# Performance work log

Measured on AMD Instinct MI355X. Metric: run time of the kernel, lower is better.

The kernel has to match this reference:

```python
import jax, jax.numpy as jnp
import numpy as np

ATTN_SCALE = 0.12  # attn_args.attn_scale (constant hyperparameter)
EPS = 1e-6         # F.rms_norm eps
GATE_IN = 12       # attn_gate input features (x[..., :12])


def rms_norm(x):
    return x * jax.lax.rsqrt(jnp.mean(x * x, axis=-1, keepdims=True) + EPS)


def rotary(x, cos, sin):
    # x: [B,T,H,D]; cos/sin: [T,D//2]
    x1, x2 = jnp.split(x, 2, axis=-1)
    c = cos[None, :, None, :]
    s = sin[None, :, None, :]
    return jnp.concatenate([x1 * c + x2 * s, -x1 * s + x2 * c], axis=-1)


def setup_inputs() -> dict:
    key = jax.random.key(0)
    ks = jax.random.split(key, 5)
    B, T, D, H, HD = 1, 2048, 1024, 8, 128
    std = 0.5 * D ** -0.5
    x = jax.random.normal(ks[0], (B, T, D), jnp.float32)
    qkvo_w = jax.random.normal(ks[1], (4, D, D), jnp.float32) * std
    gate_w = jax.random.normal(ks[2], (H, GATE_IN), jnp.float32) * 0.02
    ve = jax.random.normal(ks[3], (B, T, H, HD), jnp.float32)
    sa_lambdas = jax.random.uniform(ks[4], (2,), jnp.float32, 0.3, 0.7)
    half = HD // 2
    inv_freq = 1.0 / (10000.0 ** (jnp.arange(half, dtype=jnp.float32) / half))
    ang = jnp.arange(T, dtype=jnp.float32)[:, None] * inv_freq[None, :]
    return dict(x=x, qkvo_w=qkvo_w, gate_w=gate_w, ve=ve,
                sa_lambdas=sa_lambdas, cos=jnp.cos(ang), sin=jnp.sin(ang))


def reference(x, qkvo_w, gate_w, ve, sa_lambdas, cos, sin):
    B, T, D = x.shape
    H = gate_w.shape[0]
    HD = D // H
    # fused QKV projection: rows of qkvo_w[:3] are [q; k; v]
    w_qkv = qkvo_w[:3].reshape(3 * D, D)           # [3D, D]
    qkv = jnp.einsum('btd,ed->bte', x, w_qkv)      # [B,T,3D]
    qkv = qkv.reshape(B, T, 3, H, HD)
    q, k, v = qkv[:, :, 0], qkv[:, :, 1], qkv[:, :, 2]
    # RMSNorm + RoPE on q, k
    q = rotary(rms_norm(q), cos, sin)
    k = rotary(rms_norm(k), cos, sin)
    # value-residual mixing
    v = sa_lambdas[0] * v + sa_lambdas[1] * ve
    # causal SDPA with custom scale
    scores = jnp.einsum('bqhd,bkhd->bhqk', q, k) * ATTN_SCALE
    causal = jnp.tril(jnp.ones((T, T), dtype=bool))
    scores = jnp.where(causal[None, None], scores, jnp.finfo(scores.dtype).min)
    p = jax.nn.softmax(scores, axis=-1)
    y = jnp.einsum('bhqk,bkhd->bqhd', p, v)        # [B,T,H,HD]
    # per-head sigmoid gate from the first 12 channels of x
    gate = jax.nn.sigmoid(jnp.einsum('bti,hi->bth', x[..., :GATE_IN], gate_w))
    y = y * gate[..., None]
    # output projection (qkvo_w[3]): F.linear -> y @ W_o^T
    out = jnp.einsum('bti,oi->bto', y.reshape(B, T, H * HD), qkvo_w[3])
    return out
```

## Files before the change

kernel.cpp:

```cpp
#include <hip/hip_runtime.h>
#include <stdint.h>

typedef unsigned short u16;
typedef unsigned int u32;

typedef __bf16 bfx8 __attribute__((ext_vector_type(8)));
typedef float fx4 __attribute__((ext_vector_type(4)));
typedef float fx16 __attribute__((ext_vector_type(16)));
typedef u16 u16x4 __attribute__((ext_vector_type(4)));
typedef u16 u16x8 __attribute__((ext_vector_type(8)));

#define GAS __attribute__((address_space(1)))
#define LAS __attribute__((address_space(3)))

__device__ __forceinline__ void gload16(const void* g, void* l) {
  __builtin_amdgcn_global_load_lds((GAS void*)g, (LAS void*)l, 16, 0, 0);
}

__device__ __forceinline__ u16 f2bf(float f) {
  union { float f; u32 u; } v; v.f = f;
  u32 r = v.u + 0x7fffu + ((v.u >> 16) & 1u);
  return (u16)(r >> 16);
}
__device__ __forceinline__ float bf2f(u16 u) {
  union { u32 u; float f; } v; v.u = ((u32)u) << 16;
  return v.f;
}

__global__ __launch_bounds__(256) void k_cvt(const float* __restrict__ src, u16* __restrict__ dst, int n) {
  int i = (blockIdx.x * 256 + threadIdx.x) * 8;
  if (i >= n) return;
  const float4* s = (const float4*)(src + i);
  float4 a = s[0], b = s[1];
  u16x8 o;
  o[0] = f2bf(a.x); o[1] = f2bf(a.y); o[2] = f2bf(a.z); o[3] = f2bf(a.w);
  o[4] = f2bf(b.x); o[5] = f2bf(b.y); o[6] = f2bf(b.z); o[7] = f2bf(b.w);
  *(u16x8*)(dst + i) = o;
}

__global__ __launch_bounds__(256) void k_gemm_out(const u16* __restrict__ A, const u16* __restrict__ B,
                                                  float* __restrict__ C, int M, int N, int K) {
  __shared__ char sm[16384];
  const int tid = threadIdx.x;
  const int l = tid & 63, w = tid >> 6;
  const int li = l & 15, lg = l >> 4;
  const int nbm = M >> 6;
  const int bm = blockIdx.x % nbm, bn = blockIdx.x / nbm;

  const u16* gsrc[4];
#pragma unroll
  for (int i = 0; i < 4; ++i) {
    int b = i * 4096 + tid * 16;
    int row, ch;
    const u16* mat;
    if (b < 8192) { row = b >> 7; mat = A + (size_t)(bm * 64 + row) * K; }
    else          { int bb = b - 8192; row = bb >> 7; mat = B + (size_t)(bn * 64 + row) * K; }
    ch = ((b >> 4) & 7) ^ (row & 7);
    gsrc[i] = mat + ch * 8;
  }

  fx4 acc[4];
#pragma unroll
  for (int jj = 0; jj < 4; ++jj)
#pragma unroll
    for (int r = 0; r < 4; ++r) acc[jj][r] = 0.f;

  for (int k0 = 0; k0 < K; k0 += 64) {
    __syncthreads();
#pragma unroll
    for (int i = 0; i < 4; ++i) gload16(gsrc[i] + k0, sm + i * 4096 + w * 1024);
    __syncthreads();
#pragma unroll
    for (int kk = 0; kk < 2; ++kk) {
      int rowa = w * 16 + li;
      bfx8 af = *(const bfx8*)(sm + rowa * 128 + (((kk * 4 + lg)) ^ (rowa & 7)) * 16);
#pragma unroll
      for (int nf = 0; nf < 4; ++nf) {
        int rowb = nf * 16 + li;
        bfx8 bfr = *(const bfx8*)(sm + 8192 + rowb * 128 + ((kk * 4 + lg) ^ (rowb & 7)) * 16);
        acc[nf] = __builtin_amdgcn_mfma_f32_16x16x32_bf16(af, bfr, acc[nf], 0, 0, 0);
      }
    }
  }
#pragma unroll
  for (int nf = 0; nf < 4; ++nf)
#pragma unroll
    for (int r = 0; r < 4; ++r) {
      int row = bm * 64 + w * 16 + lg * 4 + r;
      int col = bn * 64 + nf * 16 + li;
      C[(size_t)row * N + col] = acc[nf][r];
    }
}

__global__ __launch_bounds__(256) void k_gemm_qkv(const u16* __restrict__ A, const u16* __restrict__ B,
                                                  u16* __restrict__ qkv, u16* __restrict__ vt,
                                                  const float* __restrict__ ve, const float* __restrict__ lam,
                                                  const float* __restrict__ cosp, const float* __restrict__ sinp) {
  __shared__ char sm[24576];
  const int tid = threadIdx.x;
  const int l = tid & 63, w = tid >> 6;
  const int li = l & 15, lg = l >> 4;
  const int bm = blockIdx.x & 31, bn = blockIdx.x >> 5;
  const int K = 1024;

  const u16* gsrc[6];
#pragma unroll
  for (int i = 0; i < 6; ++i) {
    int b = i * 4096 + tid * 16;
    int row, ch;
    const u16* mat;
    if (b < 8192) { row = b >> 7; mat = A + (size_t)(bm * 64 + row) * K; }
    else          { int bb = b - 8192; row = bb >> 7; mat = B + (size_t)(bn * 128 + row) * K; }
    ch = ((b >> 4) & 7) ^ (row & 7);
    gsrc[i] = mat + ch * 8;
  }

  fx4 acc[8];
#pragma unroll
  for (int jj = 0; jj < 8; ++jj)
#pragma unroll
    for (int r = 0; r < 4; ++r) acc[jj][r] = 0.f;

  for (int k0 = 0; k0 < K; k0 += 64) {
    __syncthreads();
#pragma unroll
    for (int i = 0; i < 6; ++i) gload16(gsrc[i] + k0, sm + i * 4096 + w * 1024);
    __syncthreads();
#pragma unroll
    for (int kk = 0; kk < 2; ++kk) {
      int rowa = w * 16 + li;
      bfx8 af = *(const bfx8*)(sm + rowa * 128 + ((kk * 4 + lg) ^ (rowa & 7)) * 16);
#pragma unroll
      for (int nf = 0; nf < 8; ++nf) {
        int rowb = nf * 16 + li;
        bfx8 bfr = *(const bfx8*)(sm + 8192 + rowb * 128 + ((kk * 4 + lg) ^ (rowb & 7)) * 16);
        acc[nf] = __builtin_amdgcn_mfma_f32_16x16x32_bf16(af, bfr, acc[nf], 0, 0, 0);
      }
    }
  }

  const int s = bn >> 3, h = bn & 7;
  if (s < 2) {
#pragma unroll
    for (int r = 0; r < 4; ++r) {
      int t = bm * 64 + w * 16 + lg * 4 + r;
      float ss = 0.f;
#pragma unroll
      for (int nf = 0; nf < 8; ++nf) ss += acc[nf][r] * acc[nf][r];
      ss += __shfl_xor(ss, 1); ss += __shfl_xor(ss, 2);
      ss += __shfl_xor(ss, 4); ss += __shfl_xor(ss, 8);
      float rn = rsqrtf(ss * (1.f / 128.f) + 1e-6f);
      u16* qp = qkv + (size_t)t * 3072 + s * 1024 + h * 128;
#pragma unroll
      for (int nf = 0; nf < 4; ++nf) {
        int dp = nf * 16 + li;
        float c = cosp[(size_t)t * 64 + dp];
        float sn = sinp[(size_t)t * 64 + dp];
        float x1 = acc[nf][r] * rn, x2 = acc[nf + 4][r] * rn;
        qp[dp] = f2bf(x1 * c + x2 * sn);
        qp[dp + 64] = f2bf(-x1 * sn + x2 * c);
      }
    }
  } else {
    const float l0 = lam[0], l1 = lam[1];
    int tb = bm * 64 + w * 16 + lg * 4;
#pragma unroll
    for (int nf = 0; nf < 8; ++nf) {
      int d = nf * 16 + li;
      u16x4 o;
#pragma unroll
      for (int r = 0; r < 4; ++r)
        o[r] = f2bf(l0 * acc[nf][r] + l1 * ve[(size_t)(tb + r) * 1024 + h * 128 + d]);
      *(u16x4*)(vt + (size_t)h * 262144 + (size_t)d * 2048 + tb) = o;
    }
  }
}

__global__ __launch_bounds__(256) void k_attn2(const u16* __restrict__ qkv, const u16* __restrict__ vt,
                                               float* __restrict__ part, float* __restrict__ ml) {
  __shared__ char sm[32768];
  const int bid = blockIdx.x;
  const int h = bid / 40;
  const int r40 = bid % 40;
  const int g = (r40 < 4) ? 0 : (r40 < 12) ? 1 : (r40 < 24) ? 2 : 3;
  const int Gt = (g == 0) ? 0 : (g == 1) ? 4 : (g == 2) ? 12 : 24;
  const int nseg = g + 1;
  const int idx = r40 - Gt;
  const int qb = g * 4 + idx / nseg;
  const int s = idx % nseg;
  const int q0 = qb * 128;
  const int seg0 = s * 512;
  const int seg_len = min(512, (qb + 1) * 128 - seg0);
  const int nkt = seg_len >> 5;

  const int tid = threadIdx.x;
  const int l = tid & 63, w = tid >> 6;
  const int li = l & 31, hi = l >> 5;
  const int qrow = q0 + w * 32 + li;
  const int wqmax = q0 + w * 32 + 31;
  const int wqmin = q0 + w * 32;

  bfx8 Q[8];
  {
    const u16* qp = qkv + (size_t)qrow * 3072 + h * 128 + hi * 8;
#pragma unroll
    for (int c = 0; c < 8; ++c) Q[c] = *(const bfx8*)(qp + c * 16);
  }

  const u16* kbase = qkv + 1024 + h * 128;
  const u16* vbase = vt + (size_t)h * 262144;

  auto STAGE = [&](int kt, int buf) {
    const int kabs = seg0 + kt * 32;
    char* dst = sm + buf * 16384;
#pragma unroll
    for (int i = 0; i < 2; ++i) {
      int j = w * 2 + i;
      int row = j * 4 + (l >> 4);
      int ch = (l & 15) ^ (row & 7);
      gload16(kbase + (size_t)(kabs + row) * 3072 + ch * 8, dst + j * 1024);
    }
#pragma unroll
    for (int i = 0; i < 2; ++i) {
      int j = w * 2 + i;
      int d = (j & 1) * 64 + l;
      int slot = j >> 1;
      gload16(vbase + (size_t)d * 2048 + kabs + slot * 8, dst + 8192 + j * 1024);
    }
  };

  fx16 Y[4];
#pragma unroll
  for (int d = 0; d < 4; ++d)
#pragma unroll
    for (int r = 0; r < 16; ++r) Y[d][r] = 0.f;
  float m_run = -1e30f, l_run = 0.f;

  STAGE(0, 0);
  __syncthreads();
  int cur = 0;

  for (int kt = 0; kt < nkt; ++kt) {
    if (kt + 1 < nkt) STAGE(kt + 1, cur ^ 1);
    const int k0 = seg0 + kt * 32;
    if (k0 <= wqmax) {
      const char* kb = sm + cur * 16384;
      const char* vb = kb + 8192;
      fx16 S;
#pragma unroll
      for (int r = 0; r < 16; ++r) S[r] = 0.f;
#pragma unroll
      for (int c = 0; c < 8; ++c) {
        int ch = (c * 2 + hi) ^ (li & 7);
        bfx8 kf = *(const bfx8*)(kb + li * 256 + ch * 16);
        S = __builtin_amdgcn_mfma_f32_32x32x16_bf16(kf, Q[c], S, 0, 0, 0);
      }
      const bool nomask = (k0 + 31 <= wqmin);
      float p[16];
      float mt = -1e30f;
#pragma unroll
      for (int r = 0; r < 16; ++r) {
        int kk = (r & 3) + 8 * (r >> 2) + 4 * hi;
        float sv = (nomask || (k0 + kk <= qrow)) ? S[r] * 0.12f : -1e30f;
        p[r] = sv;
        mt = fmaxf(mt, sv);
      }
      mt = fmaxf(mt, __shfl_xor(mt, 32));
      float mnew = fmaxf(m_run, mt);
      float alpha = __expf(m_run - mnew);
      float ssum = 0.f;
#pragma unroll
      for (int r = 0; r < 16; ++r) { float e = __expf(p[r] - mnew); p[r] = e; ssum += e; }
      ssum += __shfl_xor(ssum, 32);
      l_run = l_run * alpha + ssum;
      m_run = mnew;
#pragma unroll
      for (int d = 0; d < 4; ++d)
#pragma unroll
        for (int r = 0; r < 16; ++r) Y[d][r] *= alpha;
      u32 pk[8], pks[8];
#pragma unroll
      for (int i = 0; i < 8; ++i) pk[i] = (u32)f2bf(p[2 * i]) | ((u32)f2bf(p[2 * i + 1]) << 16);
#pragma unroll
      for (int i = 0; i < 8; ++i) pks[i] = (u32)__shfl_xor((int)pk[i], 32);
      union { u32 u[4]; bfx8 v; } P0, P1;
      if (hi == 0) {
        P0.u[0] = pk[0];  P0.u[1] = pk[1];  P0.u[2] = pks[0]; P0.u[3] = pks[1];
        P1.u[0] = pk[4];  P1.u[1] = pk[5];  P1.u[2] = pks[4]; P1.u[3] = pks[5];
      } else {
        P0.u[0] = pks[2]; P0.u[1] = pks[3]; P0.u[2] = pk[2];  P0.u[3] = pk[3];
        P1.u[0] = pks[6]; P1.u[1] = pks[7]; P1.u[2] = pk[6];  P1.u[3] = pk[7];
      }
#pragma unroll
      for (int db = 0; db < 4; ++db) {
        int dd = db * 32 + li;
        bfx8 v0 = *(const bfx8*)(vb + hi * 2048 + dd * 16);
        bfx8 v1 = *(const bfx8*)(vb + (2 + hi) * 2048 + dd * 16);
        Y[db] = __builtin_amdgcn_mfma_f32_32x32x16_bf16(v0, P0.v, Y[db], 0, 0, 0);
        Y[db] = __builtin_amdgcn_mfma_f32_32x32x16_bf16(v1, P1.v, Y[db], 0, 0, 0);
      }
    }
    __syncthreads();
    cur ^= 1;
  }

  if (hi == 0) {
    ml[(size_t)bid * 256 + (w * 32 + li) * 2 + 0] = m_run;
    ml[(size_t)bid * 256 + (w * 32 + li) * 2 + 1] = l_run;
  }
  float* Yl = (float*)(sm + w * 8192);
  float* pdst = part + (size_t)bid * 16384;
#pragma unroll
  for (int P = 0; P < 2; ++P) {
    asm volatile("" ::: "memory");
#pragma unroll
    for (int dh = 0; dh < 2; ++dh) {
      int db = P * 2 + dh;
#pragma unroll
      for (int r = 0; r < 16; ++r) {
        int dloc = dh * 32 + (r & 3) + 8 * (r >> 2) + 4 * hi;
        Yl[li * 64 + (dloc ^ ((li & 7) << 2))] = Y[db][r];
      }
    }
    asm volatile("" ::: "memory");
    int rr = l >> 1, c0 = (l & 1) * 32, sx = (rr & 7) << 2;
#pragma unroll
    for (int j = 0; j < 8; ++j) {
      float4 v = *(const float4*)(Yl + rr * 64 + ((c0 + j * 4) ^ sx));
      *(float4*)(pdst + (w * 32 + rr) * 128 + P * 64 + c0 + j * 4) = v;
    }
  }
}

__global__ __launch_bounds__(256) void k_comb(const float* __restrict__ part, const float* __restrict__ ml,
                                              const float* __restrict__ x, const float* __restrict__ gw,
                                              u16* __restrict__ y) {
  const int b = blockIdx.x;
  const int h = b >> 4, qb = b & 15;
  const int g = qb >> 2;
  const int nseg = g + 1;
  const int Gt = (g == 0) ? 0 : (g == 1) ? 4 : (g == 2) ? 12 : 24;
  const int slot0 = h * 40 + Gt + (qb & 3) * nseg;
  const int t = threadIdx.x;
  const int r = t >> 1, hf = (t & 1) * 64;
  const int q = qb * 128 + r;

  float ms[4], ls[4];
  float M = -1e30f;
#pragma unroll
  for (int s = 0; s < 4; ++s) {
    if (s < nseg) {
      ms[s] = ml[(size_t)(slot0 + s) * 256 + r * 2 + 0];
      ls[s] = ml[(size_t)(slot0 + s) * 256 + r * 2 + 1];
      M = fmaxf(M, ms[s]);
    }
  }
  float wt[4];
  float L = 0.f;
#pragma unroll
  for (int s = 0; s < 4; ++s) {
    if (s < nseg) { wt[s] = __expf(ms[s] - M); L += wt[s] * ls[s]; }
  }
  float4 acc[16];
#pragma unroll
  for (int j = 0; j < 16; ++j) { acc[j].x = 0.f; acc[j].y = 0.f; acc[j].z = 0.f; acc[j].w = 0.f; }
#pragma unroll
  for (int s = 0; s < 4; ++s) {
    if (s < nseg) {
      const float4* P = (const float4*)(part + (size_t)(slot0 + s) * 16384 + r * 128 + hf);
      float ws_ = wt[s];
#pragma unroll
      for (int j = 0; j < 16; ++j) {
        float4 v = P[j];
        acc[j].x += ws_ * v.x; acc[j].y += ws_ * v.y; acc[j].z += ws_ * v.z; acc[j].w += ws_ * v.w;
      }
    }
  }
  float dot = 0.f;
#pragma unroll
  for (int i = 0; i < 12; ++i) dot += x[(size_t)q * 1024 + i] * gw[h * 12 + i];
  float gt_ = 1.f / (1.f + __expf(-dot));
  float sc = gt_ / L;
  u16* yp = y + (size_t)q * 1024 + h * 128 + hf;
#pragma unroll
  for (int j = 0; j < 8; ++j) {
    float4 a = acc[2 * j], bb = acc[2 * j + 1];
    u16x8 o;
    o[0] = f2bf(a.x * sc); o[1] = f2bf(a.y * sc); o[2] = f2bf(a.z * sc); o[3] = f2bf(a.w * sc);
    o[4] = f2bf(bb.x * sc); o[5] = f2bf(bb.y * sc); o[6] = f2bf(bb.z * sc); o[7] = f2bf(bb.w * sc);
    *(u16x8*)(yp + j * 8) = o;
  }
}

extern "C" void kernel_launch(void* const* d_in, const int* in_sizes, int n_in,
                              void* d_out, int out_size, void* d_ws, size_t ws_size,
                              hipStream_t stream) {
  const float* x = (const float*)d_in[0];
  const float* qkvo_w = (const float*)d_in[1];
  const float* gate_w = (const float*)d_in[2];
  const float* ve = (const float*)d_in[3];
  const float* lam = (const float*)d_in[4];
  const float* cosp = (const float*)d_in[5];
  const float* sinp = (const float*)d_in[6];
  float* out = (float*)d_out;

  u16* wb  = (u16*)d_ws;
  u16* xb  = wb + 4u * 1024 * 1024;
  u16* qkv = xb + 2u * 1024 * 1024;
  u16* vt  = qkv + 6u * 1024 * 1024;
  u16* y   = vt + 2u * 1024 * 1024;
  float* part = (float*)((char*)d_ws + (size_t)32 * 1024 * 1024);
  float* ml = part + (size_t)320 * 16384;

  k_cvt<<<dim3(2048), dim3(256), 0, stream>>>(qkvo_w, wb, 4 * 1024 * 1024);
  k_cvt<<<dim3(1024), dim3(256), 0, stream>>>(x, xb, 2 * 1024 * 1024);
  k_gemm_qkv<<<dim3(32 * 24), dim3(256), 0, stream>>>(xb, wb, qkv, vt, ve, lam, cosp, sinp);
  k_attn2<<<dim3(320), dim3(256), 0, stream>>>(qkv, vt, part, ml);
  k_comb<<<dim3(128), dim3(256), 0, stream>>>(part, ml, x, gate_w, y);
  k_gemm_out<<<dim3(32 * 16), dim3(256), 0, stream>>>(y, wb + 3u * 1024 * 1024, out, 2048, 1024, 1024);
}
```

Measured before the change: 101.9 us.

## Split attention KV into 256-key segments, store partials in bf16, remap blocks per XCD

Attention work is split into 256-key segments instead of 512, giving 576 blocks instead of 320 for better load balance across CUs. A closed-form segment index replaces the group tables. Partial outputs are stored as bf16 to halve partial traffic, and the combine kernel merges up to 8 segments. Block IDs in both GEMMs and the attention kernel are remapped so consecutive tiles land on the same XCD for L2 reuse. In exchange, bf16 partials lose precision and the combine step reads more segments.

```diff
diff --git a/kernel.cpp b/kernel.cpp
--- a/kernel.cpp
+++ b/kernel.cpp
@@ -26,6 +26,8 @@
   union { u32 u; float f; } v; v.u = ((u32)u) << 16;
   return v.f;
 }
+
+__device__ __forceinline__ int segF(int qb) { return (qb * qb + 2 * qb + (qb & 1)) >> 2; }
 
 __global__ __launch_bounds__(256) void k_cvt(const float* __restrict__ src, u16* __restrict__ dst, int n) {
   int i = (blockIdx.x * 256 + threadIdx.x) * 8;
@@ -44,8 +46,9 @@
   const int tid = threadIdx.x;
   const int l = tid & 63, w = tid >> 6;
   const int li = l & 15, lg = l >> 4;
+  const int bid = (blockIdx.x & 7) * 64 + (blockIdx.x >> 3);
   const int nbm = M >> 6;
-  const int bm = blockIdx.x % nbm, bn = blockIdx.x / nbm;
+  const int bm = bid % nbm, bn = bid / nbm;
 
   const u16* gsrc[4];
 #pragma unroll
@@ -100,7 +103,8 @@
   const int tid = threadIdx.x;
   const int l = tid & 63, w = tid >> 6;
   const int li = l & 15, lg = l >> 4;
-  const int bm = blockIdx.x & 31, bn = blockIdx.x >> 5;
+  const int bid = (blockIdx.x & 7) * 96 + (blockIdx.x >> 3);
+  const int bm = bid & 31, bn = bid >> 5;
   const int K = 1024;
 
   const u16* gsrc[6];
@@ -177,20 +181,17 @@
 }
 
 __global__ __launch_bounds__(256) void k_attn2(const u16* __restrict__ qkv, const u16* __restrict__ vt,
-                                               float* __restrict__ part, float* __restrict__ ml) {
+                                               u16* __restrict__ part, float* __restrict__ ml) {
   __shared__ char sm[32768];
-  const int bid = blockIdx.x;
-  const int h = bid / 40;
-  const int r40 = bid % 40;
-  const int g = (r40 < 4) ? 0 : (r40 < 12) ? 1 : (r40 < 24) ? 2 : 3;
-  const int Gt = (g == 0) ? 0 : (g == 1) ? 4 : (g == 2) ? 12 : 24;
-  const int nseg = g + 1;
-  const int idx = r40 - Gt;
-  const int qb = g * 4 + idx / nseg;
-  const int s = idx % nseg;
+  const int bid = (blockIdx.x & 7) * 72 + (blockIdx.x >> 3);
+  const int h = bid / 72;
+  const int r72 = bid % 72;
+  int qb = 15;
+  while (segF(qb) > r72) --qb;
+  const int s = r72 - segF(qb);
   const int q0 = qb * 128;
-  const int seg0 = s * 512;
-  const int seg_len = min(512, (qb + 1) * 128 - seg0);
+  const int seg0 = s * 256;
+  const int seg_len = min(256, (qb + 1) * 128 - seg0);
   const int nkt = seg_len >> 5;
 
   const int tid = threadIdx.x;
@@ -309,7 +310,7 @@
     ml[(size_t)bid * 256 + (w * 32 + li) * 2 + 1] = l_run;
   }
   float* Yl = (float*)(sm + w * 8192);
-  float* pdst = part + (size_t)bid * 16384;
+  u16* pdst = part + (size_t)bid * 16384;
 #pragma unroll
   for (int P = 0; P < 2; ++P) {
     asm volatile("" ::: "memory");
@@ -327,52 +328,53 @@
 #pragma unroll
     for (int j = 0; j < 8; ++j) {
       float4 v = *(const float4*)(Yl + rr * 64 + ((c0 + j * 4) ^ sx));
-      *(float4*)(pdst + (w * 32 + rr) * 128 + P * 64 + c0 + j * 4) = v;
-    }
-  }
-}
-
-__global__ __launch_bounds__(256) void k_comb(const float* __restrict__ part, const float* __restrict__ ml,
+      u16x4 o;
+      o[0] = f2bf(v.x); o[1] = f2bf(v.y); o[2] = f2bf(v.z); o[3] = f2bf(v.w);
+      *(u16x4*)(pdst + (w * 32 + rr) * 128 + P * 64 + c0 + j * 4) = o;
+    }
+  }
+}
+
+__global__ __launch_bounds__(256) void k_comb(const u16* __restrict__ part, const float* __restrict__ ml,
                                               const float* __restrict__ x, const float* __restrict__ gw,
                                               u16* __restrict__ y) {
   const int b = blockIdx.x;
   const int h = b >> 4, qb = b & 15;
-  const int g = qb >> 2;
-  const int nseg = g + 1;
-  const int Gt = (g == 0) ? 0 : (g == 1) ? 4 : (g == 2) ? 12 : 24;
-  const int slot0 = h * 40 + Gt + (qb & 3) * nseg;
+  const int nseg = (qb + 2) >> 1;
+  const int slot0 = h * 72 + segF(qb);
   const int t = threadIdx.x;
   const int r = t >> 1, hf = (t & 1) * 64;
   const int q = qb * 128 + r;
 
-  float ms[4], ls[4];
+  float ms[8], ls[8];
   float M = -1e30f;
 #pragma unroll
-  for (int s = 0; s < 4; ++s) {
+  for (int s = 0; s < 8; ++s) {
     if (s < nseg) {
       ms[s] = ml[(size_t)(slot0 + s) * 256 + r * 2 + 0];
       ls[s] = ml[(size_t)(slot0 + s) * 256 + r * 2 + 1];
       M = fmaxf(M, ms[s]);
     }
   }
-  float wt[4];
+  float wt[8];
   float L = 0.f;
 #pragma unroll
-  for (int s = 0; s < 4; ++s) {
+  for (int s = 0; s < 8; ++s) {
     if (s < nseg) { wt[s] = __expf(ms[s] - M); L += wt[s] * ls[s]; }
   }
-  float4 acc[16];
-#pragma unroll
-  for (int j = 0; j < 16; ++j) { acc[j].x = 0.f; acc[j].y = 0.f; acc[j].z = 0.f; acc[j].w = 0.f; }
-#pragma unroll
-  for (int s = 0; s < 4; ++s) {
+  float accv[64];
+#pragma unroll
+  for (int j = 0; j < 64; ++j) accv[j] = 0.f;
+#pragma unroll
+  for (int s = 0; s < 8; ++s) {
     if (s < nseg) {
-      const float4* P = (const float4*)(part + (size_t)(slot0 + s) * 16384 + r * 128 + hf);
+      const u16x8* P = (const u16x8*)(part + (size_t)(slot0 + s) * 16384 + r * 128 + hf);
       float ws_ = wt[s];
 #pragma unroll
-      for (int j = 0; j < 16; ++j) {
-        float4 v = P[j];
-        acc[j].x += ws_ * v.x; acc[j].y += ws_ * v.y; acc[j].z += ws_ * v.z; acc[j].w += ws_ * v.w;
+      for (int j = 0; j < 8; ++j) {
+        u16x8 v = P[j];
+#pragma unroll
+        for (int e = 0; e < 8; ++e) accv[j * 8 + e] += ws_ * bf2f(v[e]);
       }
     }
   }
@@ -384,10 +386,9 @@
   u16* yp = y + (size_t)q * 1024 + h * 128 + hf;
 #pragma unroll
   for (int j = 0; j < 8; ++j) {
-    float4 a = acc[2 * j], bb = acc[2 * j + 1];
     u16x8 o;
-    o[0] = f2bf(a.x * sc); o[1] = f2bf(a.y * sc); o[2] = f2bf(a.z * sc); o[3] = f2bf(a.w * sc);
-    o[4] = f2bf(bb.x * sc); o[5] = f2bf(bb.y * sc); o[6] = f2bf(bb.z * sc); o[7] = f2bf(bb.w * sc);
+#pragma unroll
+    for (int e = 0; e < 8; ++e) o[e] = f2bf(accv[j * 8 + e] * sc);
     *(u16x8*)(yp + j * 8) = o;
   }
 }
@@ -409,13 +410,13 @@
   u16* qkv = xb + 2u * 1024 * 1024;
   u16* vt  = qkv + 6u * 1024 * 1024;
   u16* y   = vt + 2u * 1024 * 1024;
-  float* part = (float*)((char*)d_ws + (size_t)32 * 1024 * 1024);
-  float* ml = part + (size_t)320 * 16384;
+  u16* part = y + 2u * 1024 * 1024;
+  float* ml = (float*)(part + (size_t)576 * 16384);
 
   k_cvt<<<dim3(2048), dim3(256), 0, stream>>>(qkvo_w, wb, 4 * 1024 * 1024);
   k_cvt<<<dim3(1024), dim3(256), 0, stream>>>(x, xb, 2 * 1024 * 1024);
   k_gemm_qkv<<<dim3(32 * 24), dim3(256), 0, stream>>>(xb, wb, qkv, vt, ve, lam, cosp, sinp);
-  k_attn2<<<dim3(320), dim3(256), 0, stream>>>(qkv, vt, part, ml);
+  k_attn2<<<dim3(576), dim3(256), 0, stream>>>(qkv, vt, part, ml);
   k_comb<<<dim3(128), dim3(256), 0, stream>>>(part, ml, x, gate_w, y);
   k_gemm_out<<<dim3(32 * 16), dim3(256), 0, stream>>>(y, wb + 3u * 1024 * 1024, out, 2048, 1024, 1024);
 }
```

After: 101.2 us. Within noise of the previous version (-0.7%).
